# Kernel tuning notes

Measured on AMD Instinct MI355X. Metric: run time of the kernel, lower is better.

Reference implementation:

```python
import jax, jax.numpy as jnp
import numpy as np

B, S, D = 2, 2048, 1024
H, KVH, HD = 16, 4, 64


def setup_inputs() -> dict:
    key = jax.random.key(0)
    ks = jax.random.split(key, 7)
    return {
        "hidden_states": jax.random.normal(ks[0], (B, S, D), jnp.float32),
        "full_mask": jax.random.normal(ks[1], (B, 1, S, S), jnp.float32),
        "tag_mask": jax.random.normal(ks[2], (B, 1, S, S), jnp.float32),
        "wq": jax.random.normal(ks[3], (H * HD, D), jnp.float32) * 0.02,
        "wk": jax.random.normal(ks[4], (KVH * HD, D), jnp.float32) * 0.02,
        "wv": jax.random.normal(ks[5], (KVH * HD, D), jnp.float32) * 0.02,
        "wo": jax.random.normal(ks[6], (D, H * HD), jnp.float32) * 0.02,
    }


def _masked_sdpa(q, k, v, mask):
    # q,k,v: [B, h, S, HD]; mask: [B, 1, S, S] additive bias
    scale = 1.0 / jnp.sqrt(jnp.asarray(HD, q.dtype))
    w = jnp.einsum("bhqd,bhkd->bhqk", q, k) * scale + mask
    w = jax.nn.softmax(w.astype(jnp.float32), axis=-1).astype(q.dtype)
    return jnp.einsum("bhqk,bhkd->bhqd", w, v)


def _repeat_kv(x, n_rep):
    # [B, KVh, S, HD] -> [B, KVh*n_rep, S, HD]
    if n_rep == 1:
        return x
    return jnp.repeat(x, n_rep, axis=1)


def reference(hidden_states, full_mask, tag_mask, wq, wk, wv, wo):
    x = hidden_states
    q = (x @ wq.T).reshape(B, S, H, HD).transpose(0, 2, 1, 3)      # bhsd
    k = (x @ wk.T).reshape(B, S, KVH, HD).transpose(0, 2, 1, 3)
    v = (x @ wv.T).reshape(B, S, KVH, HD).transpose(0, 2, 1, 3)

    n_gq, n_lq = H // 2, H - H // 2
    n_gkv, n_lkv = KVH // 2, KVH - KVH // 2
    q_g, q_l = q[:, :n_gq], q[:, n_gq:]
    k_g, k_l = k[:, :n_gkv], k[:, n_gkv:]
    v_g, v_l = v[:, :n_gkv], v[:, n_gkv:]

    k_g = _repeat_kv(k_g, n_gq // n_gkv)
    v_g = _repeat_kv(v_g, n_gq // n_gkv)
    k_l = _repeat_kv(k_l, n_lq // n_lkv)
    v_l = _repeat_kv(v_l, n_lq // n_lkv)

    out_g = _masked_sdpa(q_g, k_g, v_g, full_mask)
    out_l = _masked_sdpa(q_l, k_l, v_l, tag_mask)
    attn = jnp.concatenate([out_g, out_l], axis=1)                  # [B,H,S,HD]
    attn = attn.transpose(0, 2, 1, 3).reshape(B, S, H * HD)
    return attn @ wo.T
```

## Files before the change

### kernel.cpp

```cpp
#include <hip/hip_runtime.h>
#include <hip/hip_bf16.h>

#define B_ 2
#define S_ 2048
#define D_ 1024
#define H_ 16
#define KVH_ 4
#define HD_ 64

#define LOG2E 1.44269504089f
#define QSCALE 0.18033688011f

#define PO_HALF ((size_t)B_ * H_ * S_ * HD_)
#define PML_HALF ((size_t)B_ * H_ * S_ * 2)

typedef __attribute__((ext_vector_type(4))) float f32x4;
typedef __attribute__((ext_vector_type(16))) float f32x16;
typedef __attribute__((ext_vector_type(8))) short short8;

#define DEV static __device__ __forceinline__

DEV unsigned short f2bf(float f) {
  union { float f; unsigned int u; } v; v.f = f;
  unsigned int r = v.u + 0x7FFFu + ((v.u >> 16) & 1u);
  return (unsigned short)(r >> 16);
}

DEV float fexp2(float x) {
#if __has_builtin(__builtin_amdgcn_exp2f)
  return __builtin_amdgcn_exp2f(x);
#else
  float r;
  asm("v_exp_f32 %0, %1" : "=v"(r) : "v"(x));
  return r;
#endif
}

DEV unsigned int pack_bf16(float lo, float hi) {
  float2 f2; f2.x = lo; f2.y = hi;
  __hip_bfloat162 h2 = __float22bfloat162_rn(f2);
  union { __hip_bfloat162 h; unsigned int u; } cv;
  cv.h = h2;
  return cv.u;
}

DEV void gload_lds16(const void* g, void* l) {
  __builtin_amdgcn_global_load_lds(
      (const __attribute__((address_space(1))) unsigned int*)g,
      (__attribute__((address_space(3))) unsigned int*)l, 16, 0, 0);
}

__global__ __launch_bounds__(256) void cast_kernel(const float* __restrict__ src,
                                                   unsigned short* __restrict__ dst, int n4) {
  int i = blockIdx.x * 256 + threadIdx.x;
  if (i >= n4) return;
  float4 v = ((const float4*)src)[i];
  ushort4 o;
  o.x = f2bf(v.x); o.y = f2bf(v.y); o.z = f2bf(v.z); o.w = f2bf(v.w);
  ((ushort4*)dst)[i] = o;
}

template <int MODE>
__global__ __launch_bounds__(256) void gemm_bt(
    const unsigned short* __restrict__ A, const unsigned short* __restrict__ Bw,
    float* __restrict__ C, unsigned short* __restrict__ qb,
    unsigned short* __restrict__ kb, unsigned short* __restrict__ vb,
    int M, int N, int K, int ntn) {
  __shared__ __align__(16) unsigned short As[128 * 64];
  __shared__ __align__(16) unsigned short Bs[128 * 64];
  const int tid = threadIdx.x;
  const int lane = tid & 63, wid = tid >> 6;
  const int wr = wid >> 1, wc = wid & 1;
  const int tm = blockIdx.x / ntn, tn = blockIdx.x % ntn;
  const int row0 = tm * 128, col0 = tn * 128;
  f32x4 acc[4][4] = {};
  const int sr = tid >> 3, sc = (tid & 7) * 8;
  for (int kt = 0; kt < K; kt += 64) {
    __syncthreads();
#pragma unroll
    for (int i = 0; i < 4; ++i) {
      gload_lds16(A + (size_t)(row0 + i * 32 + sr) * K + kt + sc,
                  (void*)(As + i * 2048 + tid * 8));
      gload_lds16(Bw + (size_t)(col0 + i * 32 + sr) * K + kt + sc,
                  (void*)(Bs + i * 2048 + tid * 8));
    }
    __syncthreads();
#pragma unroll
    for (int ks = 0; ks < 64; ks += 32) {
      const int fc = ks + (lane >> 4) * 8;
      short8 af[4], bf[4];
#pragma unroll
      for (int m = 0; m < 4; ++m)
        af[m] = *(const short8*)&As[(wr * 64 + m * 16 + (lane & 15)) * 64 + fc];
#pragma unroll
      for (int n = 0; n < 4; ++n)
        bf[n] = *(const short8*)&Bs[(wc * 64 + n * 16 + (lane & 15)) * 64 + fc];
#pragma unroll
      for (int m = 0; m < 4; ++m)
#pragma unroll
        for (int n = 0; n < 4; ++n)
          acc[m][n] = __builtin_amdgcn_mfma_f32_16x16x32_bf16(af[m], bf[n], acc[m][n], 0, 0, 0);
    }
  }
#pragma unroll
  for (int m = 0; m < 4; ++m)
#pragma unroll
    for (int n = 0; n < 4; ++n)
#pragma unroll
      for (int j = 0; j < 4; ++j) {
        const int grow = row0 + wr * 64 + m * 16 + (lane >> 4) * 4 + j;
        const int gcol = col0 + wc * 64 + n * 16 + (lane & 15);
        const float v = acc[m][n][j];
        if (MODE == 0) {
          C[(size_t)grow * N + gcol] = v;
        } else {
          const int b = grow >> 11, s = grow & 2047;
          if (gcol < 1024) {
            const int hh = gcol >> 6, d = gcol & 63;
            qb[(((size_t)b * H_ + hh) * S_ + s) * HD_ + d] = f2bf(v * QSCALE);
          } else if (gcol < 1280) {
            const int kk = (gcol - 1024) >> 6, d = gcol & 63;
            kb[(((size_t)b * KVH_ + kk) * S_ + s) * HD_ + d] = f2bf(v);
          } else {
            const int kk = (gcol - 1280) >> 6, d = gcol & 63;
            vb[(((size_t)b * KVH_ + kk) * HD_ + d) * S_ + s] = f2bf(v);
          }
        }
      }
}

__global__ __launch_bounds__(256) void attn_kernel(
    const unsigned short* __restrict__ qb, const unsigned short* __restrict__ kb,
    const unsigned short* __restrict__ vb, const float* __restrict__ fmask,
    const float* __restrict__ tmask, float* __restrict__ pO,
    float* __restrict__ pml) {
  __shared__ __align__(16) unsigned short Ks[2][64 * 64];
  __shared__ __align__(16) unsigned short Vs[2][64 * 64];
  __shared__ __align__(16) float Ms[2][32 * 64];
  const int tid = threadIdx.x;
  const int lane = tid & 63, w = tid >> 6;
  const int l31 = lane & 31, hi = lane >> 5;

  const int swz = (blockIdx.x % 8) * 128 + blockIdx.x / 8;
  const int hh = swz & 1, qt = (swz >> 1) & 63, half = (swz >> 7) & 1;
  const int g = (swz >> 8) & 1, b = swz >> 9;
  const int h = g * 8 + hh * 4 + w;
  const int kvh = g * 2 + hh;

  const unsigned short* kbase =
      kb + (((size_t)b * KVH_ + kvh) * S_ + half * 1024) * HD_;
  const unsigned short* vbase =
      vb + ((size_t)b * KVH_ + kvh) * HD_ * S_ + half * 1024;
  const float* mbase = (g ? tmask : fmask) + (size_t)b * S_ * S_ + half * 1024;

  short8 bq[4];
  {
    const unsigned short* qrow =
        qb + (((size_t)b * H_ + h) * S_ + qt * 32 + l31) * HD_;
#pragma unroll
    for (int ks = 0; ks < 4; ++ks)
      bq[ks] = *(const short8*)(qrow + ks * 16 + hi * 8);
  }

  f32x16 accO[2] = {};
  float mrow = -1e30f, lrow = 0.f;

  const int krow = tid >> 3, kblk = tid & 7;
  const int mrow_s = tid >> 4, mblk = tid & 15;

#define STAGE(KT, BUF)                                                                   \
  do {                                                                                   \
    gload_lds16(kbase + (size_t)((KT) + krow) * 64 + ((kblk ^ (krow & 7)) << 3),         \
                (void*)&Ks[BUF][tid * 8]);                                               \
    gload_lds16(kbase + (size_t)((KT) + 32 + krow) * 64 + ((kblk ^ (krow & 7)) << 3),    \
                (void*)&Ks[BUF][2048 + tid * 8]);                                        \
    gload_lds16(vbase + (size_t)krow * 2048 + (KT) + ((kblk ^ (krow & 7)) << 3),         \
                (void*)&Vs[BUF][tid * 8]);                                               \
    gload_lds16(vbase + (size_t)(32 + krow) * 2048 + (KT) + ((kblk ^ (krow & 7)) << 3),  \
                (void*)&Vs[BUF][2048 + tid * 8]);                                        \
    gload_lds16(mbase + (size_t)(qt * 32 + mrow_s) * 2048 + (KT) +                       \
                    ((mblk ^ (mrow_s & 15)) << 2),                                       \
                (void*)&Ms[BUF][tid * 4]);                                               \
    gload_lds16(mbase + (size_t)(qt * 32 + 16 + mrow_s) * 2048 + (KT) +                  \
                    ((mblk ^ (mrow_s & 15)) << 2),                                       \
                (void*)&Ms[BUF][1024 + tid * 4]);                                        \
  } while (0)

  STAGE(0, 0);
#pragma unroll 2
  for (int t = 0; t < 16; ++t) {
    const int cur = t & 1;
    if (t + 1 < 16) {
      STAGE((t + 1) * 64, cur ^ 1);
      asm volatile("s_waitcnt vmcnt(6)" ::: "memory");
    } else {
      asm volatile("s_waitcnt vmcnt(0)" ::: "memory");
    }
    __builtin_amdgcn_s_barrier();
    __builtin_amdgcn_sched_barrier(0);

    const unsigned short* ksb = Ks[cur];
    const unsigned short* vsb = Vs[cur];
    const float* msb = Ms[cur];

    f32x16 s[2] = {};
    __builtin_amdgcn_s_setprio(1);
#pragma unroll
    for (int u = 0; u < 2; ++u)
#pragma unroll
      for (int ks = 0; ks < 4; ++ks) {
        short8 ak = *(const short8*)&ksb[(u * 32 + l31) * 64 +
                                         (((ks * 2 + hi) ^ (lane & 7)) << 3)];
        s[u] = __builtin_amdgcn_mfma_f32_32x32x16_bf16(ak, bq[ks], s[u], 0, 0, 0);
      }
    __builtin_amdgcn_s_setprio(0);

    float tmax0 = -1e30f, tmax1 = -1e30f;
#pragma unroll
    for (int u = 0; u < 2; ++u)
#pragma unroll
      for (int rg = 0; rg < 4; ++rg) {
        f32x4 mk = *(const f32x4*)&msb[l31 * 64 +
                                       (((u * 8 + rg * 2 + hi) ^ (lane & 15)) << 2)];
        float v0 = fmaf(mk[0], LOG2E, s[u][rg * 4 + 0]);
        float v1 = fmaf(mk[1], LOG2E, s[u][rg * 4 + 1]);
        float v2 = fmaf(mk[2], LOG2E, s[u][rg * 4 + 2]);
        float v3 = fmaf(mk[3], LOG2E, s[u][rg * 4 + 3]);
        s[u][rg * 4 + 0] = v0;
        s[u][rg * 4 + 1] = v1;
        s[u][rg * 4 + 2] = v2;
        s[u][rg * 4 + 3] = v3;
        tmax0 = fmaxf(tmax0, fmaxf(v0, v1));
        tmax1 = fmaxf(tmax1, fmaxf(v2, v3));
      }
    float tmax = fmaxf(tmax0, tmax1);
    tmax = fmaxf(tmax, __shfl_xor(tmax, 32));

    if (__any(tmax > mrow + 11.5f)) {
      const float mnew = fmaxf(mrow, tmax);
      const float es = fexp2(mrow - mnew);
      mrow = mnew;
      lrow *= es;
#pragma unroll
      for (int r = 0; r < 16; ++r) {
        const float esb = __shfl(es, (r & 3) + 8 * (r >> 2) + 4 * hi);
        accO[0][r] *= esb;
        accO[1][r] *= esb;
      }
    }

    float rs0 = 0.f, rs1 = 0.f, rs2 = 0.f, rs3 = 0.f;
#pragma unroll
    for (int u = 0; u < 2; ++u)
#pragma unroll
      for (int r = 0; r < 16; r += 4) {
        float p0 = fexp2(s[u][r + 0] - mrow);
        float p1 = fexp2(s[u][r + 1] - mrow);
        float p2 = fexp2(s[u][r + 2] - mrow);
        float p3 = fexp2(s[u][r + 3] - mrow);
        s[u][r + 0] = p0; s[u][r + 1] = p1; s[u][r + 2] = p2; s[u][r + 3] = p3;
        rs0 += p0; rs1 += p1; rs2 += p2; rs3 += p3;
      }
    float rs = (rs0 + rs1) + (rs2 + rs3);
    rs += __shfl_xor(rs, 32);
    lrow += rs;

#pragma unroll
    for (int u = 0; u < 2; ++u) {
      unsigned int Dw[8], Sw[8];
#pragma unroll
      for (int i = 0; i < 8; ++i)
        Dw[i] = pack_bf16(s[u][2 * i], s[u][2 * i + 1]);
#pragma unroll
      for (int i = 0; i < 8; ++i)
        Sw[i] = (unsigned int)__shfl_xor((int)Dw[i], 32);
      short8 ap[2];
#pragma unroll
      for (int k2 = 0; k2 < 2; ++k2) {
        union { unsigned int wd[4]; short8 v; } cv;
        const int b0 = k2 * 4;
        cv.wd[0] = hi ? Sw[b0 + 2] : Dw[b0 + 0];
        cv.wd[1] = hi ? Sw[b0 + 3] : Dw[b0 + 1];
        cv.wd[2] = hi ? Dw[b0 + 2] : Sw[b0 + 0];
        cv.wd[3] = hi ? Dw[b0 + 3] : Sw[b0 + 1];
        ap[k2] = cv.v;
      }
      __builtin_amdgcn_s_setprio(1);
#pragma unroll
      for (int dt = 0; dt < 2; ++dt)
#pragma unroll
        for (int k2 = 0; k2 < 2; ++k2) {
          short8 bv = *(const short8*)&vsb[(dt * 32 + l31) * 64 +
                                           (((u * 4 + k2 * 2 + hi) ^ (lane & 7)) << 3)];
          accO[dt] = __builtin_amdgcn_mfma_f32_32x32x16_bf16(ap[k2], bv, accO[dt], 0, 0, 0);
        }
      __builtin_amdgcn_s_setprio(0);
    }
    __builtin_amdgcn_s_barrier();
    __builtin_amdgcn_sched_barrier(0);
  }
#undef STAGE

  float* pOh = pO + half * PO_HALF + (((size_t)b * H_ + h) * S_ + qt * 32) * HD_;
#pragma unroll
  for (int r = 0; r < 16; ++r) {
    const int crow = (r & 3) + 8 * (r >> 2) + 4 * hi;
    pOh[crow * 64 + l31] = accO[0][r];
    pOh[crow * 64 + 32 + l31] = accO[1][r];
  }
  if (hi == 0) {
    float* pmlh = pml + half * PML_HALF + (((size_t)b * H_ + h) * S_ + qt * 32 + l31) * 2;
    pmlh[0] = mrow;
    pmlh[1] = lrow;
  }
}

__global__ __launch_bounds__(256) void merge_kernel(
    const float* __restrict__ pO, const float* __restrict__ pml,
    unsigned short* __restrict__ attnb) {
  const int idx = blockIdx.x * 256 + threadIdx.x;
  const int d8 = (idx & 7) * 8;
  const int row = idx >> 3;
  const int s = row & 2047, hrow = (row >> 11) & 15, b = row >> 15;
  const float m0 = pml[(size_t)row * 2 + 0], l0 = pml[(size_t)row * 2 + 1];
  const float m1 = pml[PML_HALF + (size_t)row * 2 + 0];
  const float l1 = pml[PML_HALF + (size_t)row * 2 + 1];
  const float M = fmaxf(m0, m1);
  const float w0 = fexp2(m0 - M), w1 = fexp2(m1 - M);
  const float inv = 1.0f / (l0 * w0 + l1 * w1);
  const float a0 = w0 * inv, a1 = w1 * inv;
  const float* o0 = pO + (size_t)row * 64 + d8;
  const float* o1 = pO + PO_HALF + (size_t)row * 64 + d8;
  f32x4 x0 = *(const f32x4*)o0, x1 = *(const f32x4*)(o0 + 4);
  f32x4 y0 = *(const f32x4*)o1, y1 = *(const f32x4*)(o1 + 4);
  union { unsigned short us[8]; short8 v; } out;
#pragma unroll
  for (int j = 0; j < 4; ++j) {
    out.us[j] = f2bf(x0[j] * a0 + y0[j] * a1);
    out.us[4 + j] = f2bf(x1[j] * a0 + y1[j] * a1);
  }
  *(short8*)&attnb[(size_t)(b * S_ + s) * (H_ * HD_) + hrow * 64 + d8] = out.v;
}

extern "C" void kernel_launch(void* const* d_in, const int* in_sizes, int n_in,
                              void* d_out, int out_size, void* d_ws, size_t ws_size,
                              hipStream_t stream) {
  (void)in_sizes; (void)n_in; (void)out_size; (void)ws_size;
  const float* x = (const float*)d_in[0];
  const float* fmask = (const float*)d_in[1];
  const float* tmask = (const float*)d_in[2];
  const float* wq = (const float*)d_in[3];
  const float* wk = (const float*)d_in[4];
  const float* wv = (const float*)d_in[5];
  const float* wo = (const float*)d_in[6];

  unsigned short* ws = (unsigned short*)d_ws;
  unsigned short* xb = ws;
  unsigned short* wqkvb = xb + (size_t)4096 * 1024;
  unsigned short* wob = wqkvb + (size_t)1536 * 1024;
  unsigned short* qbuf = wob + (size_t)1024 * 1024;
  unsigned short* kbuf = qbuf + (size_t)4096 * 1024;
  unsigned short* vbuf = kbuf + (size_t)1024 * 1024;
  unsigned short* attnb = vbuf + (size_t)1024 * 1024;
  float* pO = (float*)(attnb + (size_t)4096 * 1024);
  float* pml = pO + 2 * PO_HALF;

  cast_kernel<<<4096, 256, 0, stream>>>(x, xb, 1048576);
  cast_kernel<<<1024, 256, 0, stream>>>(wq, wqkvb, 262144);
  cast_kernel<<<256, 256, 0, stream>>>(wk, wqkvb + (size_t)1024 * 1024, 65536);
  cast_kernel<<<256, 256, 0, stream>>>(wv, wqkvb + (size_t)1280 * 1024, 65536);
  cast_kernel<<<1024, 256, 0, stream>>>(wo, wob, 262144);

  gemm_bt<1><<<32 * 12, 256, 0, stream>>>(xb, wqkvb, nullptr, qbuf, kbuf, vbuf,
                                          4096, 1536, 1024, 12);
  attn_kernel<<<1024, 256, 0, stream>>>(qbuf, kbuf, vbuf, fmask, tmask, pO, pml);
  merge_kernel<<<2048, 256, 0, stream>>>(pO, pml, attnb);
  gemm_bt<0><<<32 * 8, 256, 0, stream>>>(attnb, wob, (float*)d_out,
                                         nullptr, nullptr, nullptr, 4096, 1024, 1024, 8);
}
```

Before: 160.3 us.

## Load attention mask straight to registers and use permlane32 swaps in softmax

The attention kernel no longer stages the additive mask through LDS. Each wave now prefetches its own mask rows from global memory into double-buffered registers one tile ahead, and the loop is manually unrolled by two so those register buffers alternate. The online softmax now runs per 32-column half-tile, and the cross-half max/sum reductions and the P-matrix repacking use v_permlane32_swap instead of ds_bpermute shuffles. The launch bounds ask for 3 blocks per CU. The intent is to cut LDS traffic, barriers and shuffle cost, but every wave of a block now fetches the same mask rows, so global/L2 mask traffic is four times larger, and the extra registers risk spills.

```diff
diff --git a/kernel.cpp b/kernel.cpp
--- a/kernel.cpp
+++ b/kernel.cpp
@@ -17,6 +17,7 @@
 typedef __attribute__((ext_vector_type(4))) float f32x4;
 typedef __attribute__((ext_vector_type(16))) float f32x16;
 typedef __attribute__((ext_vector_type(8))) short short8;
+typedef __attribute__((ext_vector_type(2))) unsigned int uint2v;
 
 #define DEV static __device__ __forceinline__
 
@@ -42,6 +43,37 @@
   union { __hip_bfloat162 h; unsigned int u; } cv;
   cv.h = h2;
   return cv.u;
+}
+
+DEV void permswap(unsigned int &a, unsigned int &b) {
+#if __has_builtin(__builtin_amdgcn_permlane32_swap)
+  uint2v r = __builtin_amdgcn_permlane32_swap(a, b, false, false);
+  a = r[0]; b = r[1];
+#else
+  asm("v_permlane32_swap_b32 %0, %1" : "+v"(a), "+v"(b));
+#endif
+}
+
+DEV float xhalf_max(float x) {
+  unsigned int ua = __builtin_bit_cast(unsigned int, x), ub;
+#if __has_builtin(__builtin_amdgcn_permlane32_swap)
+  uint2v r = __builtin_amdgcn_permlane32_swap(ua, ua, false, false);
+  ua = r[0]; ub = r[1];
+#else
+  asm("v_mov_b32 %1, %0\n\tv_permlane32_swap_b32 %0, %1" : "+v"(ua), "=&v"(ub));
+#endif
+  return fmaxf(__builtin_bit_cast(float, ua), __builtin_bit_cast(float, ub));
+}
+
+DEV float xhalf_sum(float x) {
+  unsigned int ua = __builtin_bit_cast(unsigned int, x), ub;
+#if __has_builtin(__builtin_amdgcn_permlane32_swap)
+  uint2v r = __builtin_amdgcn_permlane32_swap(ua, ua, false, false);
+  ua = r[0]; ub = r[1];
+#else
+  asm("v_mov_b32 %1, %0\n\tv_permlane32_swap_b32 %0, %1" : "+v"(ua), "=&v"(ub));
+#endif
+  return __builtin_bit_cast(float, ua) + __builtin_bit_cast(float, ub);
 }
 
 DEV void gload_lds16(const void* g, void* l) {
@@ -129,14 +161,13 @@
       }
 }
 
-__global__ __launch_bounds__(256) void attn_kernel(
+__global__ __launch_bounds__(256, 3) void attn_kernel(
     const unsigned short* __restrict__ qb, const unsigned short* __restrict__ kb,
     const unsigned short* __restrict__ vb, const float* __restrict__ fmask,
     const float* __restrict__ tmask, float* __restrict__ pO,
     float* __restrict__ pml) {
   __shared__ __align__(16) unsigned short Ks[2][64 * 64];
   __shared__ __align__(16) unsigned short Vs[2][64 * 64];
-  __shared__ __align__(16) float Ms[2][32 * 64];
   const int tid = threadIdx.x;
   const int lane = tid & 63, w = tid >> 6;
   const int l31 = lane & 31, hi = lane >> 5;
@@ -151,7 +182,8 @@
       kb + (((size_t)b * KVH_ + kvh) * S_ + half * 1024) * HD_;
   const unsigned short* vbase =
       vb + ((size_t)b * KVH_ + kvh) * HD_ * S_ + half * 1024;
-  const float* mbase = (g ? tmask : fmask) + (size_t)b * S_ * S_ + half * 1024;
+  const float* mline = (g ? tmask : fmask) +
+      ((size_t)b * S_ + qt * 32 + l31) * S_ + half * 1024;
 
   short8 bq[4];
   {
@@ -166,7 +198,6 @@
   float mrow = -1e30f, lrow = 0.f;
 
   const int krow = tid >> 3, kblk = tid & 7;
-  const int mrow_s = tid >> 4, mblk = tid & 15;
 
 #define STAGE(KT, BUF)                                                                   \
   do {                                                                                   \
@@ -178,127 +209,116 @@
                 (void*)&Vs[BUF][tid * 8]);                                               \
     gload_lds16(vbase + (size_t)(32 + krow) * 2048 + (KT) + ((kblk ^ (krow & 7)) << 3),  \
                 (void*)&Vs[BUF][2048 + tid * 8]);                                        \
-    gload_lds16(mbase + (size_t)(qt * 32 + mrow_s) * 2048 + (KT) +                       \
-                    ((mblk ^ (mrow_s & 15)) << 2),                                       \
-                (void*)&Ms[BUF][tid * 4]);                                               \
-    gload_lds16(mbase + (size_t)(qt * 32 + 16 + mrow_s) * 2048 + (KT) +                  \
-                    ((mblk ^ (mrow_s & 15)) << 2),                                       \
-                (void*)&Ms[BUF][1024 + tid * 4]);                                        \
   } while (0)
 
+#define MPREF(T, MK)                                                                     \
+  do {                                                                                   \
+    _Pragma("unroll")                                                                    \
+    for (int u = 0; u < 2; ++u)                                                          \
+      _Pragma("unroll")                                                                  \
+      for (int rg = 0; rg < 4; ++rg)                                                     \
+        MK[u][rg] = *(const f32x4*)&mline[(T) * 64 + u * 32 + rg * 8 + hi * 4];          \
+  } while (0)
+
+#define TILE(T, CUR, MKC, MKN)                                                           \
+  do {                                                                                   \
+    if ((T) + 1 < 16) MPREF((T) + 1, MKN);                                               \
+    __builtin_amdgcn_sched_barrier(0);                                                   \
+    if ((T) + 1 < 16) {                                                                  \
+      STAGE(((T) + 1) * 64, CUR ^ 1);                                                    \
+      asm volatile("s_waitcnt vmcnt(12)" ::: "memory");                                  \
+    } else {                                                                             \
+      asm volatile("s_waitcnt vmcnt(0)" ::: "memory");                                   \
+    }                                                                                    \
+    __builtin_amdgcn_s_barrier();                                                        \
+    __builtin_amdgcn_sched_barrier(0);                                                   \
+    const unsigned short* ksb = &Ks[CUR][0];                                             \
+    const unsigned short* vsb = &Vs[CUR][0];                                             \
+    _Pragma("unroll")                                                                    \
+    for (int u = 0; u < 2; ++u) {                                                        \
+      f32x16 s = {};                                                                     \
+      __builtin_amdgcn_s_setprio(1);                                                     \
+      _Pragma("unroll")                                                                  \
+      for (int ks = 0; ks < 4; ++ks) {                                                   \
+        short8 ak = *(const short8*)&ksb[(u * 32 + l31) * 64 +                           \
+                                         (((ks * 2 + hi) ^ (lane & 7)) << 3)];           \
+        s = __builtin_amdgcn_mfma_f32_32x32x16_bf16(ak, bq[ks], s, 0, 0, 0);             \
+      }                                                                                  \
+      __builtin_amdgcn_s_setprio(0);                                                     \
+      float tmax0 = -1e30f, tmax1 = -1e30f;                                              \
+      _Pragma("unroll")                                                                  \
+      for (int rg = 0; rg < 4; ++rg) {                                                   \
+        float v0 = fmaf(MKC[u][rg][0], LOG2E, s[rg * 4 + 0]);                            \
+        float v1 = fmaf(MKC[u][rg][1], LOG2E, s[rg * 4 + 1]);                            \
+        float v2 = fmaf(MKC[u][rg][2], LOG2E, s[rg * 4 + 2]);                            \
+        float v3 = fmaf(MKC[u][rg][3], LOG2E, s[rg * 4 + 3]);                            \
+        s[rg * 4 + 0] = v0; s[rg * 4 + 1] = v1;                                          \
+        s[rg * 4 + 2] = v2; s[rg * 4 + 3] = v3;                                          \
+        tmax0 = fmaxf(tmax0, fmaxf(v0, v1));                                             \
+        tmax1 = fmaxf(tmax1, fmaxf(v2, v3));                                             \
+      }                                                                                  \
+      float tmax = xhalf_max(fmaxf(tmax0, tmax1));                                       \
+      if (__any(tmax > mrow + 11.5f)) {                                                  \
+        const float mnew = fmaxf(mrow, tmax);                                            \
+        const float es = fexp2(mrow - mnew);                                             \
+        mrow = mnew;                                                                     \
+        lrow *= es;                                                                      \
+        _Pragma("unroll")                                                                \
+        for (int r = 0; r < 16; ++r) {                                                   \
+          const float esb = __shfl(es, (r & 3) + 8 * (r >> 2) + 4 * hi);                 \
+          accO[0][r] *= esb;                                                             \
+          accO[1][r] *= esb;                                                             \
+        }                                                                                \
+      }                                                                                  \
+      float rs0 = 0.f, rs1 = 0.f, rs2 = 0.f, rs3 = 0.f;                                  \
+      _Pragma("unroll")                                                                  \
+      for (int r = 0; r < 16; r += 4) {                                                  \
+        float p0 = fexp2(s[r + 0] - mrow);                                               \
+        float p1 = fexp2(s[r + 1] - mrow);                                               \
+        float p2 = fexp2(s[r + 2] - mrow);                                               \
+        float p3 = fexp2(s[r + 3] - mrow);                                               \
+        s[r + 0] = p0; s[r + 1] = p1; s[r + 2] = p2; s[r + 3] = p3;                      \
+        rs0 += p0; rs1 += p1; rs2 += p2; rs3 += p3;                                      \
+      }                                                                                  \
+      lrow += xhalf_sum((rs0 + rs1) + (rs2 + rs3));                                      \
+      unsigned int Dw[8];                                                                \
+      _Pragma("unroll")                                                                  \
+      for (int i = 0; i < 8; ++i)                                                        \
+        Dw[i] = pack_bf16(s[2 * i], s[2 * i + 1]);                                       \
+      permswap(Dw[0], Dw[2]); permswap(Dw[1], Dw[3]);                                    \
+      permswap(Dw[4], Dw[6]); permswap(Dw[5], Dw[7]);                                    \
+      short8 ap[2];                                                                      \
+      _Pragma("unroll")                                                                  \
+      for (int k2 = 0; k2 < 2; ++k2) {                                                   \
+        union { unsigned int wd[4]; short8 v; } cv;                                      \
+        cv.wd[0] = Dw[k2 * 4 + 0]; cv.wd[1] = Dw[k2 * 4 + 1];                            \
+        cv.wd[2] = Dw[k2 * 4 + 2]; cv.wd[3] = Dw[k2 * 4 + 3];                            \
+        ap[k2] = cv.v;                                                                   \
+      }                                                                                  \
+      __builtin_amdgcn_s_setprio(1);                                                     \
+      _Pragma("unroll")                                                                  \
+      for (int dt = 0; dt < 2; ++dt)                                                     \
+        _Pragma("unroll")                                                                \
+        for (int k2 = 0; k2 < 2; ++k2) {                                                 \
+          short8 bv = *(const short8*)&vsb[(dt * 32 + l31) * 64 +                        \
+                                           (((u * 4 + k2 * 2 + hi) ^ (lane & 7)) << 3)]; \
+          accO[dt] = __builtin_amdgcn_mfma_f32_32x32x16_bf16(ap[k2], bv, accO[dt], 0, 0, 0); \
+        }                                                                                \
+      __builtin_amdgcn_s_setprio(0);                                                     \
+    }                                                                                    \
+    __builtin_amdgcn_s_barrier();                                                        \
+    __builtin_amdgcn_sched_barrier(0);                                                   \
+  } while (0)
+
+  f32x4 mkA[2][4], mkB[2][4];
+  MPREF(0, mkA);
   STAGE(0, 0);
-#pragma unroll 2
-  for (int t = 0; t < 16; ++t) {
-    const int cur = t & 1;
-    if (t + 1 < 16) {
-      STAGE((t + 1) * 64, cur ^ 1);
-      asm volatile("s_waitcnt vmcnt(6)" ::: "memory");
-    } else {
-      asm volatile("s_waitcnt vmcnt(0)" ::: "memory");
-    }
-    __builtin_amdgcn_s_barrier();
-    __builtin_amdgcn_sched_barrier(0);
-
-    const unsigned short* ksb = Ks[cur];
-    const unsigned short* vsb = Vs[cur];
-    const float* msb = Ms[cur];
-
-    f32x16 s[2] = {};
-    __builtin_amdgcn_s_setprio(1);
-#pragma unroll
-    for (int u = 0; u < 2; ++u)
-#pragma unroll
-      for (int ks = 0; ks < 4; ++ks) {
-        short8 ak = *(const short8*)&ksb[(u * 32 + l31) * 64 +
-                                         (((ks * 2 + hi) ^ (lane & 7)) << 3)];
-        s[u] = __builtin_amdgcn_mfma_f32_32x32x16_bf16(ak, bq[ks], s[u], 0, 0, 0);
-      }
-    __builtin_amdgcn_s_setprio(0);
-
-    float tmax0 = -1e30f, tmax1 = -1e30f;
-#pragma unroll
-    for (int u = 0; u < 2; ++u)
-#pragma unroll
-      for (int rg = 0; rg < 4; ++rg) {
-        f32x4 mk = *(const f32x4*)&msb[l31 * 64 +
-                                       (((u * 8 + rg * 2 + hi) ^ (lane & 15)) << 2)];
-        float v0 = fmaf(mk[0], LOG2E, s[u][rg * 4 + 0]);
-        float v1 = fmaf(mk[1], LOG2E, s[u][rg * 4 + 1]);
-        float v2 = fmaf(mk[2], LOG2E, s[u][rg * 4 + 2]);
-        float v3 = fmaf(mk[3], LOG2E, s[u][rg * 4 + 3]);
-        s[u][rg * 4 + 0] = v0;
-        s[u][rg * 4 + 1] = v1;
-        s[u][rg * 4 + 2] = v2;
-        s[u][rg * 4 + 3] = v3;
-        tmax0 = fmaxf(tmax0, fmaxf(v0, v1));
-        tmax1 = fmaxf(tmax1, fmaxf(v2, v3));
-      }
-    float tmax = fmaxf(tmax0, tmax1);
-    tmax = fmaxf(tmax, __shfl_xor(tmax, 32));
-
-    if (__any(tmax > mrow + 11.5f)) {
-      const float mnew = fmaxf(mrow, tmax);
-      const float es = fexp2(mrow - mnew);
-      mrow = mnew;
-      lrow *= es;
-#pragma unroll
-      for (int r = 0; r < 16; ++r) {
-        const float esb = __shfl(es, (r & 3) + 8 * (r >> 2) + 4 * hi);
-        accO[0][r] *= esb;
-        accO[1][r] *= esb;
-      }
-    }
-
-    float rs0 = 0.f, rs1 = 0.f, rs2 = 0.f, rs3 = 0.f;
-#pragma unroll
-    for (int u = 0; u < 2; ++u)
-#pragma unroll
-      for (int r = 0; r < 16; r += 4) {
-        float p0 = fexp2(s[u][r + 0] - mrow);
-        float p1 = fexp2(s[u][r + 1] - mrow);
-        float p2 = fexp2(s[u][r + 2] - mrow);
-        float p3 = fexp2(s[u][r + 3] - mrow);
-        s[u][r + 0] = p0; s[u][r + 1] = p1; s[u][r + 2] = p2; s[u][r + 3] = p3;
-        rs0 += p0; rs1 += p1; rs2 += p2; rs3 += p3;
-      }
-    float rs = (rs0 + rs1) + (rs2 + rs3);
-    rs += __shfl_xor(rs, 32);
-    lrow += rs;
-
-#pragma unroll
-    for (int u = 0; u < 2; ++u) {
-      unsigned int Dw[8], Sw[8];
-#pragma unroll
-      for (int i = 0; i < 8; ++i)
-        Dw[i] = pack_bf16(s[u][2 * i], s[u][2 * i + 1]);
-#pragma unroll
-      for (int i = 0; i < 8; ++i)
-        Sw[i] = (unsigned int)__shfl_xor((int)Dw[i], 32);
-      short8 ap[2];
-#pragma unroll
-      for (int k2 = 0; k2 < 2; ++k2) {
-        union { unsigned int wd[4]; short8 v; } cv;
-        const int b0 = k2 * 4;
-        cv.wd[0] = hi ? Sw[b0 + 2] : Dw[b0 + 0];
-        cv.wd[1] = hi ? Sw[b0 + 3] : Dw[b0 + 1];
-        cv.wd[2] = hi ? Dw[b0 + 2] : Sw[b0 + 0];
-        cv.wd[3] = hi ? Dw[b0 + 3] : Sw[b0 + 1];
-        ap[k2] = cv.v;
-      }
-      __builtin_amdgcn_s_setprio(1);
-#pragma unroll
-      for (int dt = 0; dt < 2; ++dt)
-#pragma unroll
-        for (int k2 = 0; k2 < 2; ++k2) {
-          short8 bv = *(const short8*)&vsb[(dt * 32 + l31) * 64 +
-                                           (((u * 4 + k2 * 2 + hi) ^ (lane & 7)) << 3)];
-          accO[dt] = __builtin_amdgcn_mfma_f32_32x32x16_bf16(ap[k2], bv, accO[dt], 0, 0, 0);
-        }
-      __builtin_amdgcn_s_setprio(0);
-    }
-    __builtin_amdgcn_s_barrier();
-    __builtin_amdgcn_sched_barrier(0);
-  }
+  for (int tt = 0; tt < 8; ++tt) {
+    TILE(2 * tt, 0, mkA, mkB);
+    TILE(2 * tt + 1, 1, mkB, mkA);
+  }
+#undef TILE
+#undef MPREF
 #undef STAGE
 
   float* pOh = pO + half * PO_HALF + (((size_t)b * H_ + h) * S_ + qt * 32) * HD_;
```

New measurement: 207.6 us. +29.5%, slower.
